# Optimization experiments

Measured on AMD Instinct MI355X. Metric: run time of the kernel, lower is better.

Reference implementation:

```python
import jax, jax.numpy as jnp
import numpy as np

D = 9  # nodefeat_n1 = 3 (resnet feat) + 6 (pos)


def _lstm_scan(x, Wih, Whh, bih, bhh, reverse=False):
    # x: [T, B, D] -> hidden states [T, B, D]; torch gate order i,f,g,o
    B = x.shape[1]
    def step(carry, xt):
        h, c = carry
        g = xt @ Wih.T + bih + h @ Whh.T + bhh
        i = jax.nn.sigmoid(g[:, :D])
        f = jax.nn.sigmoid(g[:, D:2*D])
        gg = jnp.tanh(g[:, 2*D:3*D])
        o = jax.nn.sigmoid(g[:, 3*D:])
        c = f * c + i * gg
        h = o * jnp.tanh(c)
        return (h, c), h
    init = (jnp.zeros((B, D), x.dtype), jnp.zeros((B, D), x.dtype))
    _, hs = jax.lax.scan(step, init, x, reverse=reverse)
    return hs


def _forward(nodes_feature, pos, attmat, msg_W, msg_b, gru_Wih, gru_Whh, gru_bih, gru_bhh,
             ro1_W, ro1_b, ro2_W, ro2_b, lf_Wih, lf_Whh, lf_bih, lf_bhh,
             lb_Wih, lb_Whh, lb_bih, lb_bhh, lr1_W, lr1_b, lr2_W, lr2_b, num_rec):
    node_feat = jnp.concatenate([nodes_feature, pos], axis=-1)  # [N,T,M,D]
    N, T, M, _ = node_feat.shape
    # valid_node_num = num_rec[b, 0] in the original code
    valid = (jnp.arange(M)[None, :] < num_rec[:, 0:1]).astype(node_feat.dtype)  # [N,M]
    att = attmat * valid[:, None, None, :]  # zero out invalid source nodes q
    src = node_feat  # message sources (h_w)
    hv = node_feat   # GRU hidden (h_v)
    hidden = node_feat
    for _ in range(2):  # iterN = 2 message-passing rounds
        msg = src @ msg_W.T + msg_b                    # [N,T,M,D] message_fc
        m = jnp.einsum('btnq,btqd->btnd', att, msg)    # attention-weighted sum over q
        # single-step GRU cell (torch gate order r,z,n)
        gx = m @ gru_Wih.T + gru_bih
        gh = hv @ gru_Whh.T + gru_bhh
        r = jax.nn.sigmoid(gx[..., :D] + gh[..., :D])
        z = jax.nn.sigmoid(gx[..., D:2*D] + gh[..., D:2*D])
        n = jnp.tanh(gx[..., 2*D:] + r * gh[..., 2*D:])
        h_new = (1.0 - z) * n + z * hv
        hidden = h_new * valid[:, None, :, None]       # invalid nodes never updated -> stay zero
        src = hidden
        hv = hidden
    vmask = valid[:, None, :, None]
    # per-frame readout (pred_label0)
    p0 = jax.nn.relu(hidden @ ro1_W.T + ro1_b) @ ro2_W.T + ro2_b
    pred_label0 = p0 * vmask
    # bidirectional LSTM over time, batched over (batch, node)
    x = hidden.transpose(1, 0, 2, 3).reshape(T, N * M, D)  # [T, N*M, D]
    hf = _lstm_scan(x, lf_Wih, lf_Whh, lf_bih, lf_bhh, reverse=False)
    hb = _lstm_scan(x, lb_Wih, lb_Whh, lb_bih, lb_bhh, reverse=True)
    out = jnp.concatenate([hf, hb], axis=-1).reshape(T, N, M, 2 * D).transpose(1, 0, 2, 3)
    p = jax.nn.relu(out @ lr1_W.T + lr1_b) @ lr2_W.T + lr2_b
    pred_label = p * vmask
    return pred_label, pred_label0


def setup_inputs() -> dict:
    key = jax.random.key(0)
    ks = jax.random.split(key, 32)
    N, T, M = 8192, 20, 6
    def u(k, shape, fan_in):
        s = 1.0 / np.sqrt(fan_in).astype(np.float32)
        return jax.random.uniform(k, shape, jnp.float32, -s, s)
    return {
        "nodes_feature": jax.random.normal(ks[0], (N, T, M, 3), jnp.float32),
        "pos": jax.random.normal(ks[1], (N, T, M, 6), jnp.float32),
        "attmat": jax.random.uniform(ks[2], (N, T, M, M), jnp.float32),
        "msg_W": u(ks[3], (D, D), D), "msg_b": u(ks[4], (D,), D),
        "gru_Wih": u(ks[5], (3 * D, D), D), "gru_Whh": u(ks[6], (3 * D, D), D),
        "gru_bih": u(ks[7], (3 * D,), D), "gru_bhh": u(ks[8], (3 * D,), D),
        "ro1_W": u(ks[9], (D, D), D), "ro1_b": u(ks[10], (D,), D),
        "ro2_W": u(ks[11], (7, D), D), "ro2_b": u(ks[12], (7,), D),
        "lf_Wih": u(ks[13], (4 * D, D), D), "lf_Whh": u(ks[14], (4 * D, D), D),
        "lf_bih": u(ks[15], (4 * D,), D), "lf_bhh": u(ks[16], (4 * D,), D),
        "lb_Wih": u(ks[17], (4 * D, D), D), "lb_Whh": u(ks[18], (4 * D, D), D),
        "lb_bih": u(ks[19], (4 * D,), D), "lb_bhh": u(ks[20], (4 * D,), D),
        "lr1_W": u(ks[21], (D, 2 * D), 2 * D), "lr1_b": u(ks[22], (D,), 2 * D),
        "lr2_W": u(ks[23], (7, D), D), "lr2_b": u(ks[24], (7,), D),
        "num_rec": jax.random.randint(ks[25], (N, T), 1, M + 1),
    }


def reference(nodes_feature, pos, attmat, msg_W, msg_b, gru_Wih, gru_Whh, gru_bih, gru_bhh,
              ro1_W, ro1_b, ro2_W, ro2_b, lf_Wih, lf_Whh, lf_bih, lf_bhh,
              lb_Wih, lb_Whh, lb_bih, lb_bhh, lr1_W, lr1_b, lr2_W, lr2_b, num_rec):
    return _forward(nodes_feature, pos, attmat, msg_W, msg_b, gru_Wih, gru_Whh, gru_bih, gru_bhh,
                    ro1_W, ro1_b, ro2_W, ro2_b, lf_Wih, lf_Whh, lf_bih, lf_bhh,
                    lb_Wih, lb_Whh, lb_bih, lb_bhh, lr1_W, lr1_b, lr2_W, lr2_b, num_rec)
```

## Files before the change

### kernel.cpp

```cpp
#include <hip/hip_runtime.h>

#define N_    8192
#define T_    20
#define M_    6
#define D_    9
#define NM_   (N_*M_)
#define NT_   (N_*T_)
#define NTM7_ (N_*T_*M_*7)

#define LOG2E 1.44269504088896f

typedef __attribute__((ext_vector_type(2))) float v2f;

__device__ __forceinline__ float sigm(float x){
    return __builtin_amdgcn_rcpf(1.f + __builtin_amdgcn_exp2f(-LOG2E * x));
}
__device__ __forceinline__ float tanh_(float x){
    return fmaf(2.f, __builtin_amdgcn_rcpf(1.f + __builtin_amdgcn_exp2f(-2.f*LOG2E * x)), -1.f);
}
__device__ __forceinline__ v2f splat(float s){ return (v2f){s, s}; }
__device__ __forceinline__ v2f sigm2(v2f x){ v2f r; r.x = sigm(x.x); r.y = sigm(x.y); return r; }
__device__ __forceinline__ v2f tanh2(v2f x){ v2f r; r.x = tanh_(x.x); r.y = tanh_(x.y); return r; }
__device__ __forceinline__ v2f relu2(v2f x){ v2f r; r.x = fmaxf(x.x,0.f); r.y = fmaxf(x.y,0.f); return r; }

__global__ __launch_bounds__(64, 4) void k_fused(
    const float* __restrict__ nf,
    const float* __restrict__ pos,
    const float* __restrict__ am,
    const float* __restrict__ msgW, const float* __restrict__ msgb,
    const float* __restrict__ gWih, const float* __restrict__ gWhh,
    const float* __restrict__ gbih, const float* __restrict__ gbhh,
    const float* __restrict__ ro1W, const float* __restrict__ ro1b,
    const float* __restrict__ ro2W, const float* __restrict__ ro2b,
    const float* __restrict__ fWih, const float* __restrict__ fWhh,
    const float* __restrict__ fbih, const float* __restrict__ fbhh,
    const float* __restrict__ bWih, const float* __restrict__ bWhh,
    const float* __restrict__ bbih, const float* __restrict__ bbhh,
    const float* __restrict__ lr1W, const float* __restrict__ lr1b,
    const float* __restrict__ lr2W, const float* __restrict__ lr2b,
    const int*   __restrict__ numrec,
    float* __restrict__ out,
    float* __restrict__ out0)
{
    __shared__ float  hx[T_ * 3 * D_ * 2];
    __shared__ float4 hxs4[7 * 11];
    __shared__ v2f    shpool[1143];

    const int lane = threadIdx.x & 63;
    const int n    = blockIdx.x;

    {
        const int g    = lane / 6;
        const int i    = lane - g * 6;
        const int gB   = g * 58;
        const bool lactive = (lane < 60);

        const int wbase = n * 20;
        const int ntA = lactive ? (wbase + g)      : wbase;
        const int ntB = lactive ? (wbase + 10 + g) : wbase;
        const int nA = ntA / T_, tA = ntA - nA * T_;
        const int nB = ntB / T_, tB = ntB - nB * T_;

        v2f s[D_];
        {
            const float* pA = nf + (size_t)ntA * 18 + i * 3;
            const float* pB = nf + (size_t)ntB * 18 + i * 3;
            #pragma unroll
            for (int k = 0; k < 3; ++k) { s[k].x = pA[k]; s[k].y = pB[k]; }
        }
        {
            const float2* pA = (const float2*)(pos + (size_t)ntA * 36 + i * 6);
            const float2* pB = (const float2*)(pos + (size_t)ntB * 36 + i * 6);
            #pragma unroll
            for (int k = 0; k < 3; ++k) {
                float2 a = pA[k], b = pB[k];
                s[3 + 2*k]     = (v2f){a.x, b.x};
                s[3 + 2*k + 1] = (v2f){a.y, b.y};
            }
        }
        v2f attr[M_];
        {
            const float2* pA = (const float2*)(am + (size_t)ntA * 36 + i * 6);
            const float2* pB = (const float2*)(am + (size_t)ntB * 36 + i * 6);
            #pragma unroll
            for (int k = 0; k < 3; ++k) {
                float2 a = pA[k], b = pB[k];
                attr[2*k]     = (v2f){a.x, b.x};
                attr[2*k + 1] = (v2f){a.y, b.y};
            }
        }
        const int nrA = numrec[nA * T_];
        const int nrB = numrec[nB * T_];
        #pragma unroll
        for (int q = 0; q < M_; ++q) {
            attr[q].x *= (q < nrA) ? 1.f : 0.f;
            attr[q].y *= (q < nrB) ? 1.f : 0.f;
        }
        v2f vmi; vmi.x = (i < nrA) ? 1.f : 0.f; vmi.y = (i < nrB) ? 1.f : 0.f;

        #pragma unroll
        for (int it = 0; it < 2; ++it) {
            #pragma unroll
            for (int d = 0; d < D_; ++d) {
                v2f a = splat(msgb[d]);
                #pragma unroll
                for (int k = 0; k < D_; ++k) a += s[k] * msgW[d*9 + k];
                shpool[gB + d*6 + i] = a;
            }
            v2f mm[D_];
            #pragma unroll
            for (int d = 0; d < D_; ++d) {
                const float4* rp = (const float4*)&shpool[gB + d*6];
                float4 p0 = rp[0], p1 = rp[1], p2 = rp[2];
                v2f a = attr[0] * (v2f){p0.x, p0.y};
                a += attr[1] * (v2f){p0.z, p0.w};
                a += attr[2] * (v2f){p1.x, p1.y};
                a += attr[3] * (v2f){p1.z, p1.w};
                a += attr[4] * (v2f){p2.x, p2.y};
                a += attr[5] * (v2f){p2.z, p2.w};
                mm[d] = a;
            }
            v2f grz[18], gxn[9], ghn[9];
            #pragma unroll
            for (int j = 0; j < 18; ++j) {
                v2f a = splat(gbih[j] + gbhh[j]);
                #pragma unroll
                for (int k = 0; k < D_; ++k) {
                    a += mm[k] * gWih[j*9 + k];
                    a += s[k]  * gWhh[j*9 + k];
                }
                grz[j] = a;
            }
            #pragma unroll
            for (int j = 0; j < 9; ++j) {
                v2f ax = splat(gbih[18 + j]), ah = splat(gbhh[18 + j]);
                #pragma unroll
                for (int k = 0; k < D_; ++k) {
                    ax += mm[k] * gWih[(18 + j)*9 + k];
                    ah += s[k]  * gWhh[(18 + j)*9 + k];
                }
                gxn[j] = ax; ghn[j] = ah;
            }
            #pragma unroll
            for (int d = 0; d < D_; ++d) {
                v2f r  = sigm2(grz[d]);
                v2f z  = sigm2(grz[9 + d]);
                v2f nn = tanh2(gxn[d] + r * ghn[d]);
                s[d] = vmi * ((splat(1.f) - z) * nn + z * s[d]);
            }
        }

        if (lactive) {
            const int pr = i >> 1, par = i & 1;
            #pragma unroll
            for (int d = 0; d < D_; ++d) {
                hx[((tA*3 + pr)*9 + d)*2 + par] = s[d].x;
                hx[((tB*3 + pr)*9 + d)*2 + par] = s[d].y;
            }
        }

        v2f q9[D_];
        #pragma unroll
        for (int d = 0; d < D_; ++d) {
            v2f a = splat(ro1b[d]);
            #pragma unroll
            for (int k = 0; k < D_; ++k) a += s[k] * ro1W[d*9 + k];
            q9[d] = relu2(a);
        }
        if (lactive) {
            float* opA = out0 + (size_t)ntA * 42 + i * 7;
            float* opB = out0 + (size_t)ntB * 42 + i * 7;
            #pragma unroll
            for (int j = 0; j < 7; ++j) {
                v2f a = splat(ro2b[j]);
                #pragma unroll
                for (int k = 0; k < D_; ++k) a += q9[k] * ro2W[j*9 + k];
                a *= vmi;
                opA[j] = a.x; opB[j] = a.y;
            }
        }
    }

    __syncthreads();

    {
        int grpL = lane / 9;
        if (grpL == 7) grpL = 6;
        const int dd  = (lane == 63) ? 0 : (lane - grpL * 9);
        const bool sv   = (grpL < 6);
        const int  p    = sv ? (grpL % 3) : 0;
        const int  dir  = sv ? (grpL / 3) : 0;
        const int  xrow = grpL * 11;

        const float* Wih = dir ? bWih : fWih;
        const float* Whh = dir ? bWhh : fWhh;
        const float* Bih = dir ? bbih : fbih;
        const float* Bhh = dir ? bbhh : fbhh;

        float wxi[9], wxf[9], wxg[9], wxo[9], whi[9], whf[9], whg[9], who[9];
        #pragma unroll
        for (int k = 0; k < 9; ++k) {
            wxi[k] = Wih[(dd     )*9 + k];  whi[k] = Whh[(dd     )*9 + k];
            wxf[k] = Wih[(9  + dd)*9 + k];  whf[k] = Whh[(9  + dd)*9 + k];
            wxg[k] = Wih[(18 + dd)*9 + k];  whg[k] = Whh[(18 + dd)*9 + k];
            wxo[k] = Wih[(27 + dd)*9 + k];  who[k] = Whh[(27 + dd)*9 + k];
        }
        const float bi = Bih[dd]      + Bhh[dd];
        const float bf = Bih[9 + dd]  + Bhh[9 + dd];
        const float bg = Bih[18 + dd] + Bhh[18 + dd];
        const float bo = Bih[27 + dd] + Bhh[27 + dd];

        const int t0 = dir ? (T_ - 1) : 0;
        const int ts = dir ? -1 : 1;
        const int dir9 = dir * 9;

        {
            v2f x0 = *(const v2f*)&hx[((t0*3 + p)*9 + dd)*2];
            hxs4[xrow + dd] = make_float4(0.f, 0.f, x0.x, x0.y);
        }
        v2f h = splat(0.f), c = splat(0.f);
        for (int ss = 0; ss < T_; ++ss) {
            const int t = t0 + ts * ss;
            v2f xn = splat(0.f);
            if (ss < T_ - 1) xn = *(const v2f*)&hx[(((t + ts)*3 + p)*9 + dd)*2];

            v2f gi = splat(bi), gf = splat(bf), gg = splat(bg), go = splat(bo);
            #pragma unroll
            for (int j = 0; j < 9; ++j) {
                float4 v = hxs4[xrow + j];
                v2f hj = (v2f){v.x, v.y}, xj = (v2f){v.z, v.w};
                gi += hj * whi[j]; gi += xj * wxi[j];
                gf += hj * whf[j]; gf += xj * wxf[j];
                gg += hj * whg[j]; gg += xj * wxg[j];
                go += hj * who[j]; go += xj * wxo[j];
            }
            c = sigm2(gf) * c + sigm2(gi) * tanh2(gg);
            h = sigm2(go) * tanh2(c);
            if (sv) shpool[p*381 + t*19 + dir9 + dd] = h;
            hxs4[xrow + dd] = make_float4(h.x, h.y, xn.x, xn.y);
        }
    }

    __syncthreads();

    if (lane < 60) {
        const int pp = lane / 20;
        const int t  = lane - pp * 20;
        const int base = pp * 381 + t * 19;

        v2f hf[9], hb[9];
        #pragma unroll
        for (int k = 0; k < 9; ++k) { hf[k] = shpool[base + k]; hb[k] = shpool[base + 9 + k]; }

        const int mA2 = 2 * pp, mB2 = mA2 + 1;
        const int nr = numrec[n * T_];
        v2f vi;
        vi.x = (mA2 < nr) ? 1.f : 0.f;
        vi.y = (mB2 < nr) ? 1.f : 0.f;

        v2f q[9];
        #pragma unroll
        for (int dd2 = 0; dd2 < 9; ++dd2) {
            v2f a = splat(lr1b[dd2]);
            #pragma unroll
            for (int k = 0; k < 9; ++k) a += hf[k] * lr1W[dd2*18 + k];
            #pragma unroll
            for (int k = 0; k < 9; ++k) a += hb[k] * lr1W[dd2*18 + 9 + k];
            q[dd2] = relu2(a);
        }
        float* opA = out + (size_t)((n * T_ + t) * M_ + mA2) * 7;
        float* opB = out + (size_t)((n * T_ + t) * M_ + mB2) * 7;
        #pragma unroll
        for (int j = 0; j < 7; ++j) {
            v2f a = splat(lr2b[j]);
            #pragma unroll
            for (int k = 0; k < 9; ++k) a += q[k] * lr2W[j*9 + k];
            a *= vi;
            opA[j] = a.x; opB[j] = a.y;
        }
    }
}

extern "C" void kernel_launch(void* const* d_in, const int* in_sizes, int n_in,
                              void* d_out, int out_size, void* d_ws, size_t ws_size,
                              hipStream_t stream) {
    const float* nf    = (const float*)d_in[0];
    const float* pos   = (const float*)d_in[1];
    const float* am    = (const float*)d_in[2];
    const float* msgW  = (const float*)d_in[3];
    const float* msgb  = (const float*)d_in[4];
    const float* gWih  = (const float*)d_in[5];
    const float* gWhh  = (const float*)d_in[6];
    const float* gbih  = (const float*)d_in[7];
    const float* gbhh  = (const float*)d_in[8];
    const float* ro1W  = (const float*)d_in[9];
    const float* ro1b  = (const float*)d_in[10];
    const float* ro2W  = (const float*)d_in[11];
    const float* ro2b  = (const float*)d_in[12];
    const float* lfWih = (const float*)d_in[13];
    const float* lfWhh = (const float*)d_in[14];
    const float* lfbih = (const float*)d_in[15];
    const float* lfbhh = (const float*)d_in[16];
    const float* lbWih = (const float*)d_in[17];
    const float* lbWhh = (const float*)d_in[18];
    const float* lbbih = (const float*)d_in[19];
    const float* lbbhh = (const float*)d_in[20];
    const float* lr1W  = (const float*)d_in[21];
    const float* lr1b  = (const float*)d_in[22];
    const float* lr2W  = (const float*)d_in[23];
    const float* lr2b  = (const float*)d_in[24];
    const int* numrec  = (const int*)d_in[25];

    float* outp = (float*)d_out;
    float* out0 = (float*)d_out + NTM7_;

    k_fused<<<N_, 64, 0, stream>>>(nf, pos, am, msgW, msgb, gWih, gWhh,
                                   gbih, gbhh, ro1W, ro1b, ro2W, ro2b,
                                   lfWih, lfWhh, lfbih, lfbhh,
                                   lbWih, lbWhh, lbbih, lbbhh,
                                   lr1W, lr1b, lr2W, lr2b, numrec,
                                   outp, out0);
}
```

Baseline: 270.4 us.

## Hoist LSTM input projection off the recurrence and fuse the lr1 projection into the scan

The LSTM loop now computes the input-gate projection for the next timestep after the state update, so only the hidden-state matvec stays on the serial dependency chain. Each lane also accumulates its direction's share of the lr1 linear layer into a shared buffer during the scan, with forward and backward halves combined via assign-then-add. That shrinks the epilogue to a bias plus ReLU. Shared-memory rows are padded to 10 float2 so they can be read with wide vector loads. In exchange the loop does extra per-step LDS traffic and a read-modify-write on the shared buffer, and it relies on the single-wavefront lockstep ordering between the two directions.

```diff
diff --git a/kernel.cpp b/kernel.cpp
--- a/kernel.cpp
+++ b/kernel.cpp
@@ -22,6 +22,18 @@
 __device__ __forceinline__ v2f sigm2(v2f x){ v2f r; r.x = sigm(x.x); r.y = sigm(x.y); return r; }
 __device__ __forceinline__ v2f tanh2(v2f x){ v2f r; r.x = tanh_(x.x); r.y = tanh_(x.y); return r; }
 __device__ __forceinline__ v2f relu2(v2f x){ v2f r; r.x = fmaxf(x.x,0.f); r.y = fmaxf(x.y,0.f); return r; }
+
+#define LOADROW9(BASE, DST)                                          \
+    {                                                                \
+        const float4* _p4 = (const float4*)(BASE);                   \
+        float4 _a = _p4[0], _b = _p4[1], _c = _p4[2], _d = _p4[3];   \
+        v2f _e = (BASE)[8];                                          \
+        DST[0]=(v2f){_a.x,_a.y}; DST[1]=(v2f){_a.z,_a.w};            \
+        DST[2]=(v2f){_b.x,_b.y}; DST[3]=(v2f){_b.z,_b.w};            \
+        DST[4]=(v2f){_c.x,_c.y}; DST[5]=(v2f){_c.z,_c.w};            \
+        DST[6]=(v2f){_d.x,_d.y}; DST[7]=(v2f){_d.z,_d.w};            \
+        DST[8]=_e;                                                   \
+    }
 
 __global__ __launch_bounds__(64, 4) void k_fused(
     const float* __restrict__ nf,
@@ -42,9 +54,9 @@
     float* __restrict__ out,
     float* __restrict__ out0)
 {
-    __shared__ float  hx[T_ * 3 * D_ * 2];
-    __shared__ float4 hxs4[7 * 11];
-    __shared__ v2f    shpool[1143];
+    __shared__ v2f hxv [60 * 10];
+    __shared__ v2f hbuf[7 * 10];
+    __shared__ v2f shpool[638];
 
     const int lane = threadIdx.x & 63;
     const int n    = blockIdx.x;
@@ -152,10 +164,11 @@
 
         if (lactive) {
             const int pr = i >> 1, par = i & 1;
+            float* hxf = (float*)hxv;
             #pragma unroll
             for (int d = 0; d < D_; ++d) {
-                hx[((tA*3 + pr)*9 + d)*2 + par] = s[d].x;
-                hx[((tB*3 + pr)*9 + d)*2 + par] = s[d].y;
+                hxf[((tA*3 + pr)*10 + d)*2 + par] = s[d].x;
+                hxf[((tB*3 + pr)*10 + d)*2 + par] = s[d].y;
             }
         }
 
@@ -190,7 +203,7 @@
         const bool sv   = (grpL < 6);
         const int  p    = sv ? (grpL % 3) : 0;
         const int  dir  = sv ? (grpL / 3) : 0;
-        const int  xrow = grpL * 11;
+        const int  xrow = grpL * 10;
 
         const float* Wih = dir ? bWih : fWih;
         const float* Whh = dir ? bWhh : fWhh;
@@ -210,34 +223,72 @@
         const float bg = Bih[18 + dd] + Bhh[18 + dd];
         const float bo = Bih[27 + dd] + Bhh[27 + dd];
 
+        float w1r[9];
+        #pragma unroll
+        for (int k = 0; k < 9; ++k) w1r[k] = lr1W[dd*18 + dir*9 + k];
+
         const int t0 = dir ? (T_ - 1) : 0;
         const int ts = dir ? -1 : 1;
-        const int dir9 = dir * 9;
-
-        {
-            v2f x0 = *(const v2f*)&hx[((t0*3 + p)*9 + dd)*2];
-            hxs4[xrow + dd] = make_float4(0.f, 0.f, x0.x, x0.y);
-        }
+
+        hbuf[xrow + dd] = splat(0.f);
+
+        v2f gxi, gxf, gxg, gxo;
+        {
+            v2f xv[9]; LOADROW9(&hxv[(t0*3 + p)*10], xv);
+            gxi = splat(bi); gxf = splat(bf); gxg = splat(bg); gxo = splat(bo);
+            #pragma unroll
+            for (int j = 0; j < 9; ++j) {
+                gxi += xv[j] * wxi[j]; gxf += xv[j] * wxf[j];
+                gxg += xv[j] * wxg[j]; gxo += xv[j] * wxo[j];
+            }
+        }
+
         v2f h = splat(0.f), c = splat(0.f);
+        #pragma unroll 1
         for (int ss = 0; ss < T_; ++ss) {
-            const int t = t0 + ts * ss;
-            v2f xn = splat(0.f);
-            if (ss < T_ - 1) xn = *(const v2f*)&hx[(((t + ts)*3 + p)*9 + dd)*2];
-
-            v2f gi = splat(bi), gf = splat(bf), gg = splat(bg), go = splat(bo);
+            v2f hv[9]; LOADROW9(&hbuf[xrow], hv);
+
+            v2f gi = gxi, gf = gxf, gg = gxg, go = gxo;
             #pragma unroll
             for (int j = 0; j < 9; ++j) {
-                float4 v = hxs4[xrow + j];
-                v2f hj = (v2f){v.x, v.y}, xj = (v2f){v.z, v.w};
-                gi += hj * whi[j]; gi += xj * wxi[j];
-                gf += hj * whf[j]; gf += xj * wxf[j];
-                gg += hj * whg[j]; gg += xj * wxg[j];
-                go += hj * who[j]; go += xj * wxo[j];
-            }
+                gi += hv[j] * whi[j]; gf += hv[j] * whf[j];
+                gg += hv[j] * whg[j]; go += hv[j] * who[j];
+            }
+
+            if (ss > 0) {
+                const int tq = dir ? (20 - ss) : (ss - 1);
+                v2f qc = hv[0] * w1r[0];
+                #pragma unroll
+                for (int k = 1; k < 9; ++k) qc += hv[k] * w1r[k];
+                if (sv) {
+                    const int qa = (p*20 + tq)*10 + dd;
+                    if (ss <= 10) shpool[qa] = qc;
+                    else          shpool[qa] += qc;
+                }
+            }
+
             c = sigm2(gf) * c + sigm2(gi) * tanh2(gg);
             h = sigm2(go) * tanh2(c);
-            if (sv) shpool[p*381 + t*19 + dir9 + dd] = h;
-            hxs4[xrow + dd] = make_float4(h.x, h.y, xn.x, xn.y);
+            hbuf[xrow + dd] = h;
+
+            if (ss < T_ - 1) {
+                v2f xv[9]; LOADROW9(&hxv[((t0 + ts*(ss+1))*3 + p)*10], xv);
+                gxi = splat(bi); gxf = splat(bf); gxg = splat(bg); gxo = splat(bo);
+                #pragma unroll
+                for (int j = 0; j < 9; ++j) {
+                    gxi += xv[j] * wxi[j]; gxf += xv[j] * wxf[j];
+                    gxg += xv[j] * wxg[j]; gxo += xv[j] * wxo[j];
+                }
+            }
+        }
+
+        {
+            v2f hv[9]; LOADROW9(&hbuf[xrow], hv);
+            const int tq = dir ? 0 : 19;
+            v2f qc = hv[0] * w1r[0];
+            #pragma unroll
+            for (int k = 1; k < 9; ++k) qc += hv[k] * w1r[k];
+            if (sv) shpool[(p*20 + tq)*10 + dd] += qc;
         }
     }
 
@@ -246,11 +297,12 @@
     if (lane < 60) {
         const int pp = lane / 20;
         const int t  = lane - pp * 20;
-        const int base = pp * 381 + t * 19;
-
-        v2f hf[9], hb[9];
-        #pragma unroll
-        for (int k = 0; k < 9; ++k) { hf[k] = shpool[base + k]; hb[k] = shpool[base + 9 + k]; }
+
+        v2f qv[9]; LOADROW9(&shpool[(pp*20 + t)*10], qv);
+        v2f q[9];
+        #pragma unroll
+        for (int dd2 = 0; dd2 < 9; ++dd2)
+            q[dd2] = relu2(qv[dd2] + splat(lr1b[dd2]));
 
         const int mA2 = 2 * pp, mB2 = mA2 + 1;
         const int nr = numrec[n * T_];
@@ -258,16 +310,6 @@
         vi.x = (mA2 < nr) ? 1.f : 0.f;
         vi.y = (mB2 < nr) ? 1.f : 0.f;
 
-        v2f q[9];
-        #pragma unroll
-        for (int dd2 = 0; dd2 < 9; ++dd2) {
-            v2f a = splat(lr1b[dd2]);
-            #pragma unroll
-            for (int k = 0; k < 9; ++k) a += hf[k] * lr1W[dd2*18 + k];
-            #pragma unroll
-            for (int k = 0; k < 9; ++k) a += hb[k] * lr1W[dd2*18 + 9 + k];
-            q[dd2] = relu2(a);
-        }
         float* opA = out + (size_t)((n * T_ + t) * M_ + mA2) * 7;
         float* opB = out + (size_t)((n * T_ + t) * M_ + mB2) * 7;
         #pragma unroll
```

Result: slower. 916.7 us (+239.0%).

## Fold first LSTM readout layer into the recurrent loop via per-lane partial sums

Applied to the files above, without the earlier changes.

Each LSTM lane now also accumulates its share of the lr1 projection (h dot lr1W row) inside the time loop, reusing the hidden values it already reads from shared memory. Forward and backward partial sums are combined in a smaller shared buffer, so the readout phase only adds the bias and applies relu instead of doing a full 18x9 matvec. It also drops the occupancy hint from launch bounds and pins the time loop to no unrolling. The change relies on the forward and backward directions writing the same slot in a safe order (the ss<=10 store versus accumulate split), which adds a possible race and extra register pressure on the serial recurrence.

```diff
diff --git a/kernel.cpp b/kernel.cpp
--- a/kernel.cpp
+++ b/kernel.cpp
@@ -23,7 +23,7 @@
 __device__ __forceinline__ v2f tanh2(v2f x){ v2f r; r.x = tanh_(x.x); r.y = tanh_(x.y); return r; }
 __device__ __forceinline__ v2f relu2(v2f x){ v2f r; r.x = fmaxf(x.x,0.f); r.y = fmaxf(x.y,0.f); return r; }
 
-__global__ __launch_bounds__(64, 4) void k_fused(
+__global__ __launch_bounds__(64) void k_fused(
     const float* __restrict__ nf,
     const float* __restrict__ pos,
     const float* __restrict__ am,
@@ -44,7 +44,7 @@
 {
     __shared__ float  hx[T_ * 3 * D_ * 2];
     __shared__ float4 hxs4[7 * 11];
-    __shared__ v2f    shpool[1143];
+    __shared__ v2f    shpool[640];
 
     const int lane = threadIdx.x & 63;
     const int n    = blockIdx.x;
@@ -210,21 +210,26 @@
         const float bg = Bih[18 + dd] + Bhh[18 + dd];
         const float bo = Bih[27 + dd] + Bhh[27 + dd];
 
+        float w1r[9];
+        #pragma unroll
+        for (int k = 0; k < 9; ++k) w1r[k] = lr1W[dd*18 + dir*9 + k];
+
         const int t0 = dir ? (T_ - 1) : 0;
         const int ts = dir ? -1 : 1;
-        const int dir9 = dir * 9;
 
         {
             v2f x0 = *(const v2f*)&hx[((t0*3 + p)*9 + dd)*2];
             hxs4[xrow + dd] = make_float4(0.f, 0.f, x0.x, x0.y);
         }
         v2f h = splat(0.f), c = splat(0.f);
+        #pragma unroll 1
         for (int ss = 0; ss < T_; ++ss) {
             const int t = t0 + ts * ss;
             v2f xn = splat(0.f);
             if (ss < T_ - 1) xn = *(const v2f*)&hx[(((t + ts)*3 + p)*9 + dd)*2];
 
             v2f gi = splat(bi), gf = splat(bf), gg = splat(bg), go = splat(bo);
+            v2f qc = splat(0.f);
             #pragma unroll
             for (int j = 0; j < 9; ++j) {
                 float4 v = hxs4[xrow + j];
@@ -233,11 +238,32 @@
                 gf += hj * whf[j]; gf += xj * wxf[j];
                 gg += hj * whg[j]; gg += xj * wxg[j];
                 go += hj * who[j]; go += xj * wxo[j];
-            }
+                qc += hj * w1r[j];
+            }
+
+            if (ss > 0 && sv) {
+                const int tq = dir ? (20 - ss) : (ss - 1);
+                const int qa = (p*20 + tq)*10 + dd;
+                if (ss <= 10) shpool[qa] = qc;
+                else          shpool[qa] += qc;
+            }
+
             c = sigm2(gf) * c + sigm2(gi) * tanh2(gg);
             h = sigm2(go) * tanh2(c);
-            if (sv) shpool[p*381 + t*19 + dir9 + dd] = h;
             hxs4[xrow + dd] = make_float4(h.x, h.y, xn.x, xn.y);
+        }
+
+        {
+            v2f qc = splat(0.f);
+            #pragma unroll
+            for (int j = 0; j < 9; ++j) {
+                float4 v = hxs4[xrow + j];
+                qc += (v2f){v.x, v.y} * w1r[j];
+            }
+            if (sv) {
+                const int tq = dir ? 0 : 19;
+                shpool[(p*20 + tq)*10 + dd] += qc;
+            }
         }
     }
 
@@ -246,11 +272,12 @@
     if (lane < 60) {
         const int pp = lane / 20;
         const int t  = lane - pp * 20;
-        const int base = pp * 381 + t * 19;
-
-        v2f hf[9], hb[9];
-        #pragma unroll
-        for (int k = 0; k < 9; ++k) { hf[k] = shpool[base + k]; hb[k] = shpool[base + 9 + k]; }
+        const v2f* qrow = &shpool[(pp*20 + t)*10];
+
+        v2f q[9];
+        #pragma unroll
+        for (int dd2 = 0; dd2 < 9; ++dd2)
+            q[dd2] = relu2(qrow[dd2] + splat(lr1b[dd2]));
 
         const int mA2 = 2 * pp, mB2 = mA2 + 1;
         const int nr = numrec[n * T_];
@@ -258,16 +285,6 @@
         vi.x = (mA2 < nr) ? 1.f : 0.f;
         vi.y = (mB2 < nr) ? 1.f : 0.f;
 
-        v2f q[9];
-        #pragma unroll
-        for (int dd2 = 0; dd2 < 9; ++dd2) {
-            v2f a = splat(lr1b[dd2]);
-            #pragma unroll
-            for (int k = 0; k < 9; ++k) a += hf[k] * lr1W[dd2*18 + k];
-            #pragma unroll
-            for (int k = 0; k < 9; ++k) a += hb[k] * lr1W[dd2*18 + 9 + k];
-            q[dd2] = relu2(a);
-        }
         float* opA = out + (size_t)((n * T_ + t) * M_ + mA2) * 7;
         float* opB = out + (size_t)((n * T_ + t) * M_ + mB2) * 7;
         #pragma unroll
```

Measured after the change: 267.4 us. No clear change (-1.1%).
